# Optimization experiments

Measured on AMD Instinct MI355X. Metric: run time of the kernel, lower is better.

The kernel has to match this reference:

```python
import jax, jax.numpy as jnp
import numpy as np

HIDDEN = 2048
HEADS = 16
HEAD_DIM = HIDDEN // HEADS  # 128
SCALE = 1.0 / np.sqrt(HEAD_DIM).astype(np.float32)


def setup_inputs() -> dict:
    key = jax.random.key(0)
    k1, k2, k3, k4, k5 = jax.random.split(key, 5)
    B, QL = 8, 1024
    NB, BS = 32, 128  # num_blocks, block_size -> kv_len = 4096
    query = jax.random.normal(k1, (B, QL, HIDDEN), dtype=jnp.float32)
    kv_k = jax.random.normal(k2, (NB, BS, HIDDEN), dtype=jnp.float32)
    kv_v = jax.random.normal(k3, (NB, BS, HIDDEN), dtype=jnp.float32)
    # nn.Linear(bias=False) weights: y = x @ W.T
    Wq = jax.random.normal(k4, (HIDDEN, HIDDEN), dtype=jnp.float32) * (1.0 / np.sqrt(HIDDEN))
    Wo = jax.random.normal(k5, (HIDDEN, HIDDEN), dtype=jnp.float32) * (1.0 / np.sqrt(HIDDEN))
    return {"query": query, "kv_k": kv_k, "kv_v": kv_v, "Wq": Wq, "Wo": Wo}


def reference(query, kv_k, kv_v, Wq, Wo):
    # query: [B, QL, H*D]; kv_k/kv_v: [NB, BS, H*D] (shared across batch,
    # NOT re-projected in the paged path, matching the torch module).
    B, QL, _ = query.shape
    NB, BS, _ = kv_k.shape
    KV = NB * BS
    Q = (query @ Wq.T).reshape(B, QL, HEADS, HEAD_DIM)          # bqhd
    K = kv_k.reshape(KV, HEADS, HEAD_DIM)                        # khd
    V = kv_v.reshape(KV, HEADS, HEAD_DIM)
    # Blockwise online-softmax over equal blocks == one stable softmax over kv.
    scores = jnp.einsum("bqhd,khd->bhqk", Q, K) * SCALE          # [B,H,QL,KV]
    attn = jax.nn.softmax(scores, axis=-1)
    out = jnp.einsum("bhqk,khd->bqhd", attn, V).reshape(B, QL, HIDDEN)
    return out @ Wo.T
```

## Files before the change

kernel.cpp:

```cpp
#include <hip/hip_runtime.h>

#define HIDDEN 2048
#define HEADS 16
#define HDIM 128
#define BQ 8
#define QLEN 1024
#define KVLEN 4096
#define MROWS (BQ * QLEN)

typedef __bf16 bf16x8 __attribute__((ext_vector_type(8)));
typedef float f32x4 __attribute__((ext_vector_type(4)));
typedef unsigned short u16;
typedef u16 u16x8 __attribute__((ext_vector_type(8)));
typedef float f32x8v __attribute__((ext_vector_type(8)));

__device__ __forceinline__ u16 f2bf(float f) {
  union { float f; unsigned u; } v; v.f = f;
  unsigned r = (v.u + 0x7FFFu + ((v.u >> 16) & 1u)) >> 16;
  return (u16)r;
}

__device__ __forceinline__ void async_ld16(const void* g, void* l) {
  __builtin_amdgcn_global_load_lds(
      (const __attribute__((address_space(1))) void*)g,
      (__attribute__((address_space(3))) void*)l, 16, 0, 0);
}

__global__ void convert_bf16(const float* __restrict__ src, u16* __restrict__ dst,
                             long n) {
  long base = ((long)blockIdx.x * blockDim.x + threadIdx.x) * 8;
  long stride = (long)gridDim.x * blockDim.x * 8;
  for (long i = base; i < n; i += stride) {
    f32x8v s = *(const f32x8v*)(src + i);
    u16x8 o;
#pragma unroll
    for (int j = 0; j < 8; j++) o[j] = f2bf(s[j]);
    *(u16x8*)(dst + i) = o;
  }
}

__global__ __launch_bounds__(256) void transpose_v(const float* __restrict__ V,
                                                   u16* __restrict__ Vt) {
  __shared__ u16 T[128][129];
  const int kv0 = blockIdx.x * 128;
  const int h = blockIdx.y;
  const int tid = threadIdx.x;
#pragma unroll
  for (int p = 0; p < 8; p++) {
    int idx = p * 2048 + tid * 8;
    int r = idx >> 7, c = idx & 127;
    f32x8v s = *(const f32x8v*)(V + (size_t)(kv0 + r) * HIDDEN + h * HDIM + c);
#pragma unroll
    for (int j = 0; j < 8; j++) T[r][c + j] = f2bf(s[j]);
  }
  __syncthreads();
#pragma unroll
  for (int p = 0; p < 8; p++) {
    int idx = p * 2048 + tid * 8;
    int d = idx >> 7, kv = idx & 127;
    u16x8 o;
#pragma unroll
    for (int j = 0; j < 8; j++) o[j] = T[kv + j][d];
    *(u16x8*)(Vt + ((size_t)h * HDIM + d) * KVLEN + kv0 + kv) = o;
  }
}

__global__ __launch_bounds__(256) void gemm_bt(
    const u16* __restrict__ A, const u16* __restrict__ Bt, void* __restrict__ C,
    int M, int N, int K, int outf) {
  __shared__ __align__(16) u16 Asm[4 * 128 * 8];
  __shared__ __align__(16) u16 Bsm[4 * 128 * 8];
  const int tid = threadIdx.x;
  const int wid = tid >> 6, lane = tid & 63;
  const int quad = lane >> 4, l15 = lane & 15;
  const int wm = wid >> 1, wn = wid & 1;
  const int lin = blockIdx.y * gridDim.x + blockIdx.x;
  const int cpx = (gridDim.x * gridDim.y) >> 3;
  const int swz = (lin & 7) * cpx + (lin >> 3);
  const int by = swz / gridDim.x;
  const int bx = swz - by * gridDim.x;
  const int row0 = by * 128;
  const int col0 = bx * 128;

  f32x4 acc[4][4];
#pragma unroll
  for (int i = 0; i < 4; i++)
#pragma unroll
    for (int j = 0; j < 4; j++) acc[i][j] = (f32x4){0.f, 0.f, 0.f, 0.f};

  for (int k0 = 0; k0 < K; k0 += 32) {
    __syncthreads();
#pragma unroll
    for (int i = 0; i < 4; i++) {
      int seg = wid + 4 * i;
      int isB = seg >> 3;
      int s = seg & 7;
      int q = s >> 1, hv = s & 1;
      const u16* gsrc = isB ? Bt : A;
      int grow = (isB ? col0 : row0) + hv * 64 + lane;
      const u16* g = gsrc + (size_t)grow * K + (k0 + q * 8);
      u16* l = (isB ? Bsm : Asm) + (q * 128 + hv * 64) * 8;
      async_ld16(g, l);
    }
    __syncthreads();
    bf16x8 af[4], bfr[4];
#pragma unroll
    for (int mt = 0; mt < 4; mt++)
      af[mt] = *(const bf16x8*)(Asm + (quad * 128 + wm * 64 + mt * 16 + l15) * 8);
#pragma unroll
    for (int nt = 0; nt < 4; nt++)
      bfr[nt] = *(const bf16x8*)(Bsm + (quad * 128 + wn * 64 + nt * 16 + l15) * 8);
#pragma unroll
    for (int mt = 0; mt < 4; mt++)
#pragma unroll
      for (int nt = 0; nt < 4; nt++)
        acc[mt][nt] = __builtin_amdgcn_mfma_f32_16x16x32_bf16(af[mt], bfr[nt], acc[mt][nt], 0, 0, 0);
  }

#pragma unroll
  for (int mt = 0; mt < 4; mt++)
#pragma unroll
    for (int r = 0; r < 4; r++) {
      int row = row0 + wm * 64 + mt * 16 + quad * 4 + r;
#pragma unroll
      for (int nt = 0; nt < 4; nt++) {
        int col = col0 + wn * 64 + nt * 16 + l15;
        if (outf) {
          ((float*)C)[(size_t)row * N + col] = acc[mt][nt][r];
        } else {
          ((u16*)C)[(size_t)row * N + col] = f2bf(acc[mt][nt][r]);
        }
      }
    }
}

__global__ __launch_bounds__(512, 4) void attn(
    const u16* __restrict__ Q,
    const u16* __restrict__ Kv,
    const u16* __restrict__ Vt,
    u16* __restrict__ O) {
  __shared__ __align__(16) u16 KVb[16 * 1024];
  __shared__ __align__(16) u16 Pb[128 * 136];
  const int tid = threadIdx.x;
  const int wid = tid >> 6, lane = tid & 63;
  const int quad = lane >> 4, l15 = lane & 15;
  const int lin = blockIdx.x + (blockIdx.y << 3) + (blockIdx.z << 7);
  const int swz = ((lin & 7) << 7) + (lin >> 3);
  const int h = swz >> 6, b = (swz >> 3) & 7, qt = swz & 7;
  const int qrow0 = b * QLEN + qt * 128;
  const int hcol = h * HDIM;
  const float cexp = 0.08838834764831845f * 1.4426950408889634f;

  bf16x8 qf[4];
#pragma unroll
  for (int ks = 0; ks < 4; ks++) {
    int row = qrow0 + wid * 16 + l15;
    qf[ks] = *(const bf16x8*)(Q + (size_t)row * HIDDEN + hcol + ks * 32 + quad * 8);
  }

  f32x4 o[8];
#pragma unroll
  for (int dt = 0; dt < 8; dt++) o[dt] = (f32x4){0.f, 0.f, 0.f, 0.f};
  float mrun[4], lrun[4];
#pragma unroll
  for (int r = 0; r < 4; r++) { mrun[r] = -INFINITY; lrun[r] = 0.f; }

  for (int kv0 = 0; kv0 < KVLEN; kv0 += 128) {
    __syncthreads();
#pragma unroll
    for (int i = 0; i < 4; i++) {
      int seg = wid + 8 * i;
      int ch = seg >> 1, sh = seg & 1;
      int kvr = kv0 + sh * 64 + lane;
      const u16* g = Kv + (size_t)kvr * HIDDEN + hcol + ch * 8;
      async_ld16(g, KVb + (ch * 128 + sh * 64) * 8);
    }
    __syncthreads();

    f32x4 sc[8];
#pragma unroll
    for (int nt = 0; nt < 8; nt++) sc[nt] = (f32x4){0.f, 0.f, 0.f, 0.f};
#pragma unroll
    for (int ks = 0; ks < 4; ks++) {
      bf16x8 kf[8];
#pragma unroll
      for (int nt = 0; nt < 8; nt++)
        kf[nt] = *(const bf16x8*)(KVb + ((ks * 4 + quad) * 128 + nt * 16 + l15) * 8);
#pragma unroll
      for (int nt = 0; nt < 8; nt++)
        sc[nt] = __builtin_amdgcn_mfma_f32_16x16x32_bf16(qf[ks], kf[nt], sc[nt], 0, 0, 0);
    }
    __syncthreads();

#pragma unroll
    for (int i = 0; i < 4; i++) {
      int seg = wid + 8 * i;
      int ch = seg >> 1, dh = seg & 1;
      int d = dh * 64 + lane;
      const u16* g = Vt + ((size_t)hcol + d) * KVLEN + kv0 + ch * 8;
      async_ld16(g, KVb + (ch * 128 + dh * 64) * 8);
    }

#pragma unroll
    for (int r = 0; r < 4; r++) {
      float mx = sc[0][r];
#pragma unroll
      for (int nt = 1; nt < 8; nt++) mx = fmaxf(mx, sc[nt][r]);
#pragma unroll
      for (int off = 1; off < 16; off <<= 1) mx = fmaxf(mx, __shfl_xor(mx, off, 64));
      float mn = fmaxf(mrun[r], mx);
      float al = __builtin_amdgcn_exp2f((mrun[r] - mn) * cexp);
      mrun[r] = mn;
      float mc = mn * cexp;
      float ps = 0.f;
#pragma unroll
      for (int nt = 0; nt < 8; nt++) {
        float p = __builtin_amdgcn_exp2f(sc[nt][r] * cexp - mc);
        sc[nt][r] = p;
        ps += p;
      }
#pragma unroll
      for (int off = 1; off < 16; off <<= 1) ps += __shfl_xor(ps, off, 64);
      lrun[r] = lrun[r] * al + ps;
#pragma unroll
      for (int dt = 0; dt < 8; dt++) o[dt][r] *= al;
    }

#pragma unroll
    for (int nt = 0; nt < 8; nt++)
#pragma unroll
      for (int r = 0; r < 4; r++) {
        int prow = wid * 16 + quad * 4 + r;
        Pb[prow * 136 + nt * 16 + l15] = f2bf(sc[nt][r]);
      }
    __syncthreads();

#pragma unroll
    for (int ks = 0; ks < 4; ks++) {
      bf16x8 pf, vf[8];
      pf = *(const bf16x8*)(Pb + (wid * 16 + l15) * 136 + ks * 32 + quad * 8);
#pragma unroll
      for (int dt = 0; dt < 8; dt++)
        vf[dt] = *(const bf16x8*)(KVb + ((ks * 4 + quad) * 128 + dt * 16 + l15) * 8);
#pragma unroll
      for (int dt = 0; dt < 8; dt++)
        o[dt] = __builtin_amdgcn_mfma_f32_16x16x32_bf16(pf, vf[dt], o[dt], 0, 0, 0);
    }
  }

#pragma unroll
  for (int r = 0; r < 4; r++) {
    float inv = 1.0f / lrun[r];
    int row = qrow0 + wid * 16 + quad * 4 + r;
#pragma unroll
    for (int dt = 0; dt < 8; dt++) {
      int col = hcol + dt * 16 + l15;
      O[(size_t)row * HIDDEN + col] = f2bf(o[dt][r] * inv);
    }
  }
}

extern "C" void kernel_launch(void* const* d_in, const int* in_sizes, int n_in,
                              void* d_out, int out_size, void* d_ws, size_t ws_size,
                              hipStream_t stream) {
  const float* query = (const float*)d_in[0];
  const float* kv_k  = (const float*)d_in[1];
  const float* kv_v  = (const float*)d_in[2];
  const float* Wq    = (const float*)d_in[3];
  const float* Wo    = (const float*)d_in[4];
  float* out = (float*)d_out;

  const long NQ = (long)MROWS * HIDDEN;
  const long NK = (long)KVLEN * HIDDEN;
  const long NW = (long)HIDDEN * HIDDEN;

  dim3 blk(256);

  u16* convQ  = (u16*)d_ws;
  u16* convK  = convQ + NQ;
  u16* Vtb    = convK + NK;
  u16* convWq = Vtb + NK;
  u16* convWo = convWq + NW;
  u16* Qws    = convWo + NW;
  u16* Ows    = convQ;

  convert_bf16<<<dim3((NQ / 8 + 255) / 256), blk, 0, stream>>>(query, convQ,  NQ);
  convert_bf16<<<dim3((NK / 8 + 255) / 256), blk, 0, stream>>>(kv_k,  convK,  NK);
  transpose_v<<<dim3(KVLEN / 128, HEADS), blk, 0, stream>>>(kv_v, Vtb);
  convert_bf16<<<dim3((NW / 8 + 255) / 256), blk, 0, stream>>>(Wq,    convWq, NW);
  convert_bf16<<<dim3((NW / 8 + 255) / 256), blk, 0, stream>>>(Wo,    convWo, NW);

  gemm_bt<<<dim3(HIDDEN / 128, MROWS / 128), blk, 0, stream>>>(convQ, convWq, Qws, MROWS, HIDDEN, HIDDEN, 0);
  attn<<<dim3(QLEN / 128, HEADS, BQ), dim3(512), 0, stream>>>(Qws, convK, Vtb, Ows);
  gemm_bt<<<dim3(HIDDEN / 128, MROWS / 128), blk, 0, stream>>>(Ows, convWo, out, MROWS, HIDDEN, HIDDEN, 1);
}
```

Baseline: 1.042 ms.

## Use lazy softmax rescaling, native bf16 conversion, and split fragment loads

The attention kernel now rescales the running max, sum and output accumulators only when some row's new max exceeds the running max by more than a threshold, which drops most per-tile exp and multiply work on the output registers. The manual float-to-bf16 rounding helper is replaced by the compiler's native __bf16 conversion, which can map to hardware conversion instructions. K and V fragment loads are split into two halves of four, which lowers peak register pressure and lets loads interleave with MFMAs. Lazy rescaling lets exponentials grow up to about 2^8 before renormalizing, which is safe in fp32 but changes rounding slightly, and it adds a wave-wide vote branch.

```diff
diff --git a/kernel.cpp b/kernel.cpp
--- a/kernel.cpp
+++ b/kernel.cpp
@@ -14,12 +14,6 @@
 typedef u16 u16x8 __attribute__((ext_vector_type(8)));
 typedef float f32x8v __attribute__((ext_vector_type(8)));
 
-__device__ __forceinline__ u16 f2bf(float f) {
-  union { float f; unsigned u; } v; v.f = f;
-  unsigned r = (v.u + 0x7FFFu + ((v.u >> 16) & 1u)) >> 16;
-  return (u16)r;
-}
-
 __device__ __forceinline__ void async_ld16(const void* g, void* l) {
   __builtin_amdgcn_global_load_lds(
       (const __attribute__((address_space(1))) void*)g,
@@ -32,16 +26,16 @@
   long stride = (long)gridDim.x * blockDim.x * 8;
   for (long i = base; i < n; i += stride) {
     f32x8v s = *(const f32x8v*)(src + i);
-    u16x8 o;
-#pragma unroll
-    for (int j = 0; j < 8; j++) o[j] = f2bf(s[j]);
-    *(u16x8*)(dst + i) = o;
+    bf16x8 o;
+#pragma unroll
+    for (int j = 0; j < 8; j++) o[j] = (__bf16)s[j];
+    *(bf16x8*)(dst + i) = o;
   }
 }
 
 __global__ __launch_bounds__(256) void transpose_v(const float* __restrict__ V,
                                                    u16* __restrict__ Vt) {
-  __shared__ u16 T[128][129];
+  __shared__ __bf16 T[128][129];
   const int kv0 = blockIdx.x * 128;
   const int h = blockIdx.y;
   const int tid = threadIdx.x;
@@ -51,17 +45,17 @@
     int r = idx >> 7, c = idx & 127;
     f32x8v s = *(const f32x8v*)(V + (size_t)(kv0 + r) * HIDDEN + h * HDIM + c);
 #pragma unroll
-    for (int j = 0; j < 8; j++) T[r][c + j] = f2bf(s[j]);
+    for (int j = 0; j < 8; j++) T[r][c + j] = (__bf16)s[j];
   }
   __syncthreads();
 #pragma unroll
   for (int p = 0; p < 8; p++) {
     int idx = p * 2048 + tid * 8;
     int d = idx >> 7, kv = idx & 127;
-    u16x8 o;
+    bf16x8 o;
 #pragma unroll
     for (int j = 0; j < 8; j++) o[j] = T[kv + j][d];
-    *(u16x8*)(Vt + ((size_t)h * HDIM + d) * KVLEN + kv0 + kv) = o;
+    *(bf16x8*)(Vt + ((size_t)h * HDIM + d) * KVLEN + kv0 + kv) = o;
   }
 }
 
@@ -128,7 +122,7 @@
         if (outf) {
           ((float*)C)[(size_t)row * N + col] = acc[mt][nt][r];
         } else {
-          ((u16*)C)[(size_t)row * N + col] = f2bf(acc[mt][nt][r]);
+          ((__bf16*)C)[(size_t)row * N + col] = (__bf16)acc[mt][nt][r];
         }
       }
     }
@@ -140,7 +134,7 @@
     const u16* __restrict__ Vt,
     u16* __restrict__ O) {
   __shared__ __align__(16) u16 KVb[16 * 1024];
-  __shared__ __align__(16) u16 Pb[128 * 136];
+  __shared__ __align__(16) __bf16 Pb[128 * 136];
   const int tid = threadIdx.x;
   const int wid = tid >> 6, lane = tid & 63;
   const int quad = lane >> 4, l15 = lane & 15;
@@ -182,13 +176,16 @@
     for (int nt = 0; nt < 8; nt++) sc[nt] = (f32x4){0.f, 0.f, 0.f, 0.f};
 #pragma unroll
     for (int ks = 0; ks < 4; ks++) {
-      bf16x8 kf[8];
-#pragma unroll
-      for (int nt = 0; nt < 8; nt++)
-        kf[nt] = *(const bf16x8*)(KVb + ((ks * 4 + quad) * 128 + nt * 16 + l15) * 8);
-#pragma unroll
-      for (int nt = 0; nt < 8; nt++)
-        sc[nt] = __builtin_amdgcn_mfma_f32_16x16x32_bf16(qf[ks], kf[nt], sc[nt], 0, 0, 0);
+#pragma unroll
+      for (int hf = 0; hf < 2; hf++) {
+        bf16x8 kf[4];
+#pragma unroll
+        for (int j = 0; j < 4; j++)
+          kf[j] = *(const bf16x8*)(KVb + ((ks * 4 + quad) * 128 + (hf * 4 + j) * 16 + l15) * 8);
+#pragma unroll
+        for (int j = 0; j < 4; j++)
+          sc[hf * 4 + j] = __builtin_amdgcn_mfma_f32_16x16x32_bf16(qf[ks], kf[j], sc[hf * 4 + j], 0, 0, 0);
+      }
     }
     __syncthreads();
 
@@ -201,17 +198,32 @@
       async_ld16(g, KVb + (ch * 128 + dh * 64) * 8);
     }
 
+    float mx[4];
 #pragma unroll
     for (int r = 0; r < 4; r++) {
-      float mx = sc[0][r];
-#pragma unroll
-      for (int nt = 1; nt < 8; nt++) mx = fmaxf(mx, sc[nt][r]);
-#pragma unroll
-      for (int off = 1; off < 16; off <<= 1) mx = fmaxf(mx, __shfl_xor(mx, off, 64));
-      float mn = fmaxf(mrun[r], mx);
-      float al = __builtin_amdgcn_exp2f((mrun[r] - mn) * cexp);
-      mrun[r] = mn;
-      float mc = mn * cexp;
+      float m = sc[0][r];
+#pragma unroll
+      for (int nt = 1; nt < 8; nt++) m = fmaxf(m, sc[nt][r]);
+#pragma unroll
+      for (int off = 1; off < 16; off <<= 1) m = fmaxf(m, __shfl_xor(m, off, 64));
+      mx[r] = m;
+    }
+    float gmax = fmaxf(fmaxf(mx[0] - mrun[0], mx[1] - mrun[1]),
+                       fmaxf(mx[2] - mrun[2], mx[3] - mrun[3]));
+    if (__any(gmax > 8.f)) {
+#pragma unroll
+      for (int r = 0; r < 4; r++) {
+        float mn = fmaxf(mrun[r], mx[r]);
+        float al = __builtin_amdgcn_exp2f((mrun[r] - mn) * cexp);
+        mrun[r] = mn;
+        lrun[r] *= al;
+#pragma unroll
+        for (int dt = 0; dt < 8; dt++) o[dt][r] *= al;
+      }
+    }
+#pragma unroll
+    for (int r = 0; r < 4; r++) {
+      float mc = mrun[r] * cexp;
       float ps = 0.f;
 #pragma unroll
       for (int nt = 0; nt < 8; nt++) {
@@ -221,9 +233,7 @@
       }
 #pragma unroll
       for (int off = 1; off < 16; off <<= 1) ps += __shfl_xor(ps, off, 64);
-      lrun[r] = lrun[r] * al + ps;
-#pragma unroll
-      for (int dt = 0; dt < 8; dt++) o[dt][r] *= al;
+      lrun[r] += ps;
     }
 
 #pragma unroll
@@ -231,20 +241,23 @@
 #pragma unroll
       for (int r = 0; r < 4; r++) {
         int prow = wid * 16 + quad * 4 + r;
-        Pb[prow * 136 + nt * 16 + l15] = f2bf(sc[nt][r]);
+        Pb[prow * 136 + nt * 16 + l15] = (__bf16)sc[nt][r];
       }
     __syncthreads();
 
 #pragma unroll
     for (int ks = 0; ks < 4; ks++) {
-      bf16x8 pf, vf[8];
-      pf = *(const bf16x8*)(Pb + (wid * 16 + l15) * 136 + ks * 32 + quad * 8);
-#pragma unroll
-      for (int dt = 0; dt < 8; dt++)
-        vf[dt] = *(const bf16x8*)(KVb + ((ks * 4 + quad) * 128 + dt * 16 + l15) * 8);
-#pragma unroll
-      for (int dt = 0; dt < 8; dt++)
-        o[dt] = __builtin_amdgcn_mfma_f32_16x16x32_bf16(pf, vf[dt], o[dt], 0, 0, 0);
+      bf16x8 pf = *(const bf16x8*)(Pb + (wid * 16 + l15) * 136 + ks * 32 + quad * 8);
+#pragma unroll
+      for (int hf = 0; hf < 2; hf++) {
+        bf16x8 vf[4];
+#pragma unroll
+        for (int j = 0; j < 4; j++)
+          vf[j] = *(const bf16x8*)(KVb + ((ks * 4 + quad) * 128 + (hf * 4 + j) * 16 + l15) * 8);
+#pragma unroll
+        for (int j = 0; j < 4; j++)
+          o[hf * 4 + j] = __builtin_amdgcn_mfma_f32_16x16x32_bf16(pf, vf[j], o[hf * 4 + j], 0, 0, 0);
+      }
     }
   }
 
@@ -255,7 +268,7 @@
 #pragma unroll
     for (int dt = 0; dt < 8; dt++) {
       int col = hcol + dt * 16 + l15;
-      O[(size_t)row * HIDDEN + col] = f2bf(o[dt][r] * inv);
+      ((__bf16*)O)[(size_t)row * HIDDEN + col] = (__bf16)(o[dt][r] * inv);
     }
   }
 }
```

Result: faster. 956.1 us (-8.3%).
